# Kernel optimization log

Measured on AMD Instinct MI355X. Metric: run time of the kernel, lower is better.

The kernel has to match this reference:

```python
import jax, jax.numpy as jnp
import numpy as np

N_WIN = 232
T = 8
KERNEL = (2, 2, 2)
STRIDE = (2, 2, 2)
SLOPE = 25.0  # fast_sigmoid surrogate slope


@jax.custom_vjp
def spike(v):
    # heaviside(v) with fast-sigmoid surrogate gradient
    return (v > 0).astype(v.dtype)

def _spike_fwd(v):
    return spike(v), v

def _spike_bwd(v, g):
    return (g / (SLOPE * jnp.abs(v) + 1.0) ** 2,)

spike.defvjp(_spike_fwd, _spike_bwd)


def _avg_pool3d(x, kernel, stride):
    # x: (B, C, D, H, W), VALID pooling
    win = (1, 1) + tuple(kernel)
    st = (1, 1) + tuple(stride)
    s = jax.lax.reduce_window(x, 0.0, jax.lax.add, win, st, 'VALID')
    return s / float(np.prod(kernel))


def setup_inputs() -> dict:
    key = jax.random.key(0)
    ks = jax.random.split(key, 14)
    B, C, H, W = 64, 3, 32, 32
    input_dim, h0, h1, n_cls = 256, 256, 128, 6
    x = jax.random.normal(ks[0], (B, C, N_WIN, H, W), jnp.float32)
    W_in = jax.random.normal(ks[1], (h0, input_dim), jnp.float32) * 0.05
    b_in = jnp.zeros((h0,), jnp.float32)
    W_hid = jax.random.normal(ks[2], (h1, h0), jnp.float32) * 0.05
    b_hid = jnp.zeros((h1,), jnp.float32)
    in_feat = C * h1 * 14  # C * hidden[1] * D'
    W_out = jax.random.normal(ks[3], (n_cls, in_feat), jnp.float32) * 0.05
    b_out = jnp.zeros((n_cls,), jnp.float32)
    beta_in = jax.random.uniform(ks[4], (h0,), jnp.float32)
    thr_in = jax.random.uniform(ks[5], (h0,), jnp.float32)
    beta_hid = jax.random.uniform(ks[6], (h1,), jnp.float32)
    thr_hid = jax.random.uniform(ks[7], (h1,), jnp.float32)
    beta_out = jax.random.uniform(ks[8], (n_cls,), jnp.float32)
    return dict(x=x, W_in=W_in, b_in=b_in, W_hid=W_hid, b_hid=b_hid,
                W_out=W_out, b_out=b_out, beta_in=beta_in, thr_in=thr_in,
                beta_hid=beta_hid, thr_hid=thr_hid, beta_out=beta_out)


def _lif(mem, cur, beta, thr):
    # snntorch Leaky, reset-by-subtract; reset uses detached prev-mem spike
    reset = jax.lax.stop_gradient((mem > thr).astype(mem.dtype))
    mem = jnp.clip(beta, 0.0, 1.0) * mem + cur - reset * thr
    spk = spike(mem - thr)
    return spk, mem


def reference(x, W_in, b_in, W_hid, b_hid, W_out, b_out,
              beta_in, thr_in, beta_hid, thr_hid, beta_out):
    B, C, _, H, W = x.shape
    chunk = N_WIN // T  # 29
    # split depth into T chunks: (T, B, C, chunk, H, W)
    xt = x.reshape(B, C, T, chunk, H, W).transpose(2, 0, 1, 3, 4, 5)
    pooled = jax.vmap(lambda v: _avg_pool3d(v, KERNEL, STRIDE))(xt)  # (T,B,C,D',H',W')
    _, _, _, Dp, Hp, Wp = pooled.shape
    pr = pooled.reshape(T, B, C * Dp, Hp * Wp)
    # fc_in applied to all timesteps at once (recurrence-free)
    cur_in_all = jnp.einsum('tbnf,hf->tbnh', pr, W_in) + b_in  # (T,B,N,h0)

    h0 = W_in.shape[0]
    h1 = W_hid.shape[0]
    n_cls = W_out.shape[0]
    N = C * Dp
    mem_in0 = jnp.zeros((B, N, h0), x.dtype)
    mem_hid0 = jnp.zeros((B, N, h1), x.dtype)
    mem_out0 = jnp.zeros((B, n_cls), x.dtype)

    def step(carry, cur_in):
        mem_in, mem_hid, mem_out = carry
        spk_in, mem_in = _lif(mem_in, cur_in, beta_in, thr_in)
        cur_hid = jnp.einsum('bnh,gh->bng', spk_in, W_hid) + b_hid
        spk_hid, mem_hid = _lif(mem_hid, cur_hid, beta_hid, thr_hid)
        flat = spk_hid.reshape(spk_hid.shape[0], -1)  # (B, N*h1)
        cur_out = flat @ W_out.T + b_out
        spk_out, mem_out = _lif(mem_out, cur_out, beta_out, jnp.float32(1.0))
        return (mem_in, mem_hid, mem_out), spk_out

    _, spk_rec = jax.lax.scan(step, (mem_in0, mem_hid0, mem_out0), cur_in_all)
    return spk_rec  # (T, B, n_classes)
```

## Files before the change

kernel.cpp:

```cpp
#include <hip/hip_runtime.h>

#define T_STEPS 8
#define NROW    42
#define BN      2688
#define H0      256
#define H1      128
#define NCLS    6
#define KFLAT   5376

__global__ __launch_bounds__(256) void pool_kernel(const float* __restrict__ x,
                                                   float* __restrict__ pr) {
    int idx = blockIdx.x * 256 + threadIdx.x;
    int f   = idx & 255;
    int wp  = f & 15, hp = f >> 4;
    int rest = idx >> 8;
    int dp = rest % 14;
    int r2 = rest / 14;
    int c  = r2 % 3;
    int r3 = r2 / 3;
    int b  = r3 & 63;
    int t  = r3 >> 6;
    const float* base = x + ((long)b * 712704 + (long)c * 237568
                          + (long)(t * 29 + 2 * dp) * 1024
                          + (2 * hp) * 32 + 2 * wp);
    float2 v0 = *(const float2*)(base);
    float2 v1 = *(const float2*)(base + 32);
    float2 v2 = *(const float2*)(base + 1024);
    float2 v3 = *(const float2*)(base + 1056);
    float s = v0.x + v0.y + v1.x + v1.y + v2.x + v2.y + v3.x + v3.y;
    int m = t * BN + b * NROW + c * 14 + dp;
    pr[(long)m * 256 + f] = s * 0.125f;
}

__global__ __launch_bounds__(256) void gemm_abt(const float* __restrict__ A,
                                                const float* __restrict__ B,
                                                const float* __restrict__ bias,
                                                float* __restrict__ C,
                                                int N, int K) {
    __shared__ float At[16][68];
    __shared__ float Bt[16][68];
    int tid = threadIdx.x;
    int m0 = blockIdx.y * 64, n0 = blockIdx.x * 64;
    int lr = tid >> 2;
    int lq = tid & 3;
    int tm = tid & 15, tn = tid >> 4;
    float acc[4][4] = {};
    const float* Ap = A + (long)(m0 + lr) * K + lq * 4;
    const float* Bp = B + (long)(n0 + lr) * K + lq * 4;
    for (int k0 = 0; k0 < K; k0 += 16) {
        float4 a = *(const float4*)(Ap + k0);
        float4 b = *(const float4*)(Bp + k0);
        __syncthreads();
        At[lq * 4 + 0][lr] = a.x; At[lq * 4 + 1][lr] = a.y;
        At[lq * 4 + 2][lr] = a.z; At[lq * 4 + 3][lr] = a.w;
        Bt[lq * 4 + 0][lr] = b.x; Bt[lq * 4 + 1][lr] = b.y;
        Bt[lq * 4 + 2][lr] = b.z; Bt[lq * 4 + 3][lr] = b.w;
        __syncthreads();
#pragma unroll
        for (int k = 0; k < 16; ++k) {
            float4 av = *(const float4*)&At[k][tm * 4];
            float4 bv = *(const float4*)&Bt[k][tn * 4];
            float am[4] = {av.x, av.y, av.z, av.w};
            float bn_[4] = {bv.x, bv.y, bv.z, bv.w};
#pragma unroll
            for (int i = 0; i < 4; ++i)
#pragma unroll
                for (int j = 0; j < 4; ++j)
                    acc[i][j] = fmaf(am[i], bn_[j], acc[i][j]);
        }
    }
#pragma unroll
    for (int i = 0; i < 4; ++i) {
        int row = m0 + tm * 4 + i;
        int col = n0 + tn * 4;
        float4 o;
        o.x = acc[i][0] + bias[col + 0];
        o.y = acc[i][1] + bias[col + 1];
        o.z = acc[i][2] + bias[col + 2];
        o.w = acc[i][3] + bias[col + 3];
        *(float4*)&C[(long)row * N + col] = o;
    }
}

__global__ __launch_bounds__(256) void lif_kernel(const float* __restrict__ cur_all,
                                                  const float* __restrict__ beta,
                                                  const float* __restrict__ thr,
                                                  float* __restrict__ spk_all,
                                                  int F) {
    int j = blockIdx.x * 256 + threadIdx.x;
    int h = j & (F - 1);
    float be = fminf(fmaxf(beta[h], 0.f), 1.f);
    float th = thr[h];
    float mem = 0.f;
    long stride = (long)BN * F;
#pragma unroll
    for (int t = 0; t < T_STEPS; ++t) {
        float cur = cur_all[t * stride + j];
        float reset = (mem > th) ? th : 0.f;
        mem = be * mem + cur - reset;
        spk_all[t * stride + j] = ((mem - th) > 0.f) ? 1.f : 0.f;
    }
}

__global__ __launch_bounds__(256) void out_gemm(const float* __restrict__ spkh,
                                                const float* __restrict__ W_out,
                                                const float* __restrict__ b_out,
                                                float* __restrict__ cur_out) {
    __shared__ float part[256][8];
    int row = blockIdx.x;
    int tid = threadIdx.x;
    const float* a = spkh + (long)row * KFLAT;
    float acc[6] = {0.f, 0.f, 0.f, 0.f, 0.f, 0.f};
    for (int j = tid; j < KFLAT; j += 256) {
        float s = a[j];
#pragma unroll
        for (int c = 0; c < 6; ++c)
            acc[c] = fmaf(s, W_out[c * KFLAT + j], acc[c]);
    }
#pragma unroll
    for (int c = 0; c < 6; ++c) part[tid][c] = acc[c];
    __syncthreads();
    for (int off = 128; off > 0; off >>= 1) {
        if (tid < off) {
#pragma unroll
            for (int c = 0; c < 6; ++c) part[tid][c] += part[tid + off][c];
        }
        __syncthreads();
    }
    if (tid < 6) cur_out[row * 6 + tid] = part[0][tid] + b_out[tid];
}

__global__ void lif_out_kernel(const float* __restrict__ cur_out,
                               const float* __restrict__ beta_out,
                               float* __restrict__ out) {
    int j = threadIdx.x;
    if (j >= 384) return;
    int cls = j % 6;
    float be = fminf(fmaxf(beta_out[cls], 0.f), 1.f);
    float mem = 0.f;
#pragma unroll
    for (int t = 0; t < T_STEPS; ++t) {
        float cur = cur_out[t * 384 + j];
        float reset = (mem > 1.f) ? 1.f : 0.f;
        mem = be * mem + cur - reset;
        out[t * 384 + j] = ((mem - 1.f) > 0.f) ? 1.f : 0.f;
    }
}

extern "C" void kernel_launch(void* const* d_in, const int* in_sizes, int n_in,
                              void* d_out, int out_size, void* d_ws, size_t ws_size,
                              hipStream_t stream) {
    (void)in_sizes; (void)n_in; (void)out_size; (void)ws_size;
    const float* x        = (const float*)d_in[0];
    const float* W_in     = (const float*)d_in[1];
    const float* b_in     = (const float*)d_in[2];
    const float* W_hid    = (const float*)d_in[3];
    const float* b_hid    = (const float*)d_in[4];
    const float* W_out    = (const float*)d_in[5];
    const float* b_out    = (const float*)d_in[6];
    const float* beta_in  = (const float*)d_in[7];
    const float* thr_in   = (const float*)d_in[8];
    const float* beta_hid = (const float*)d_in[9];
    const float* thr_hid  = (const float*)d_in[10];
    const float* beta_out = (const float*)d_in[11];
    float* out = (float*)d_out;

    float* buf0 = (float*)d_ws;
    float* buf1 = buf0 + 5505024;
    float* curo = buf1 + 5505024;

    pool_kernel<<<21504, 256, 0, stream>>>(x, buf0);
    gemm_abt<<<dim3(4, 336), 256, 0, stream>>>(buf0, W_in, b_in, buf1, 256, 256);
    lif_kernel<<<2688, 256, 0, stream>>>(buf1, beta_in, thr_in, buf0, 256);
    gemm_abt<<<dim3(2, 336), 256, 0, stream>>>(buf0, W_hid, b_hid, buf1, 128, 256);
    lif_kernel<<<1344, 256, 0, stream>>>(buf1, beta_hid, thr_hid, buf0, 128);
    out_gemm<<<512, 256, 0, stream>>>(buf0, W_out, b_out, curo);
    lif_out_kernel<<<1, 384, 0, stream>>>(curo, beta_out, out);
}
```

Baseline: 377.1 us.

## Enlarge GEMM tiles to 128x128 with 8x8 register blocking and swizzled LDS

The shared fp32 GEMM used for fc_in and fc_hid now computes 128x128 output tiles per block, with each thread holding an 8x8 accumulator instead of 4x4. Each LDS element is therefore reused more per load, reducing shared-memory traffic per FMA. A small row swizzle in LDS is added to avoid bank conflicts on the transposed stores, and launch_bounds requests 4 blocks per CU. The cost is far fewer blocks: 336 for the first GEMM and only 168 for the second, which may underfill the GPU. The 64-entry accumulator also raises register pressure.

New measurement: 402.1 us. +6.6%, slower.

```diff
diff --git a/kernel.cpp b/kernel.cpp
--- a/kernel.cpp
+++ b/kernel.cpp
@@ -7,6 +7,9 @@
 #define H1      128
 #define NCLS    6
 #define KFLAT   5376
+
+#define SW(r)   ((r) + ((r) >> 5) * 4)
+#define LDR     140
 
 __global__ __launch_bounds__(256) void pool_kernel(const float* __restrict__ x,
                                                    float* __restrict__ pr) {
@@ -32,53 +35,74 @@
     pr[(long)m * 256 + f] = s * 0.125f;
 }
 
-__global__ __launch_bounds__(256) void gemm_abt(const float* __restrict__ A,
-                                                const float* __restrict__ B,
-                                                const float* __restrict__ bias,
-                                                float* __restrict__ C,
-                                                int N, int K) {
-    __shared__ float At[16][68];
-    __shared__ float Bt[16][68];
+__global__ __launch_bounds__(256, 4) void gemm_abt(const float* __restrict__ A,
+                                                   const float* __restrict__ B,
+                                                   const float* __restrict__ bias,
+                                                   float* __restrict__ C,
+                                                   int N, int K) {
+    __shared__ float At[16 * LDR];
+    __shared__ float Bt[16 * LDR];
     int tid = threadIdx.x;
-    int m0 = blockIdx.y * 64, n0 = blockIdx.x * 64;
-    int lr = tid >> 2;
-    int lq = tid & 3;
+    int m0 = blockIdx.y * 128, n0 = blockIdx.x * 128;
+
+    int sr = tid >> 1, sq = tid & 1;
+    int scol = SW(sr);
+    const float* Ap = A + (long)(m0 + sr) * K + sq * 8;
+    const float* Bp = B + (long)(n0 + sr) * K + sq * 8;
+
     int tm = tid & 15, tn = tid >> 4;
-    float acc[4][4] = {};
-    const float* Ap = A + (long)(m0 + lr) * K + lq * 4;
-    const float* Bp = B + (long)(n0 + lr) * K + lq * 4;
+    int ca = SW(tm * 8);
+    int cb = SW(tn * 8);
+
+    float acc[8][8] = {};
+
     for (int k0 = 0; k0 < K; k0 += 16) {
-        float4 a = *(const float4*)(Ap + k0);
-        float4 b = *(const float4*)(Bp + k0);
+        float4 a0 = *(const float4*)(Ap + k0);
+        float4 a1 = *(const float4*)(Ap + k0 + 4);
+        float4 b0 = *(const float4*)(Bp + k0);
+        float4 b1 = *(const float4*)(Bp + k0 + 4);
         __syncthreads();
-        At[lq * 4 + 0][lr] = a.x; At[lq * 4 + 1][lr] = a.y;
-        At[lq * 4 + 2][lr] = a.z; At[lq * 4 + 3][lr] = a.w;
-        Bt[lq * 4 + 0][lr] = b.x; Bt[lq * 4 + 1][lr] = b.y;
-        Bt[lq * 4 + 2][lr] = b.z; Bt[lq * 4 + 3][lr] = b.w;
+        int kb = sq * 8;
+        At[(kb + 0) * LDR + scol] = a0.x; At[(kb + 1) * LDR + scol] = a0.y;
+        At[(kb + 2) * LDR + scol] = a0.z; At[(kb + 3) * LDR + scol] = a0.w;
+        At[(kb + 4) * LDR + scol] = a1.x; At[(kb + 5) * LDR + scol] = a1.y;
+        At[(kb + 6) * LDR + scol] = a1.z; At[(kb + 7) * LDR + scol] = a1.w;
+        Bt[(kb + 0) * LDR + scol] = b0.x; Bt[(kb + 1) * LDR + scol] = b0.y;
+        Bt[(kb + 2) * LDR + scol] = b0.z; Bt[(kb + 3) * LDR + scol] = b0.w;
+        Bt[(kb + 4) * LDR + scol] = b1.x; Bt[(kb + 5) * LDR + scol] = b1.y;
+        Bt[(kb + 6) * LDR + scol] = b1.z; Bt[(kb + 7) * LDR + scol] = b1.w;
         __syncthreads();
 #pragma unroll
         for (int k = 0; k < 16; ++k) {
-            float4 av = *(const float4*)&At[k][tm * 4];
-            float4 bv = *(const float4*)&Bt[k][tn * 4];
-            float am[4] = {av.x, av.y, av.z, av.w};
-            float bn_[4] = {bv.x, bv.y, bv.z, bv.w};
-#pragma unroll
-            for (int i = 0; i < 4; ++i)
-#pragma unroll
-                for (int j = 0; j < 4; ++j)
+            float4 av0 = *(const float4*)&At[k * LDR + ca];
+            float4 av1 = *(const float4*)&At[k * LDR + ca + 4];
+            float4 bv0 = *(const float4*)&Bt[k * LDR + cb];
+            float4 bv1 = *(const float4*)&Bt[k * LDR + cb + 4];
+            float am[8] = {av0.x, av0.y, av0.z, av0.w, av1.x, av1.y, av1.z, av1.w};
+            float bn_[8] = {bv0.x, bv0.y, bv0.z, bv0.w, bv1.x, bv1.y, bv1.z, bv1.w};
+#pragma unroll
+            for (int i = 0; i < 8; ++i)
+#pragma unroll
+                for (int j = 0; j < 8; ++j)
                     acc[i][j] = fmaf(am[i], bn_[j], acc[i][j]);
         }
     }
-#pragma unroll
-    for (int i = 0; i < 4; ++i) {
-        int row = m0 + tm * 4 + i;
-        int col = n0 + tn * 4;
-        float4 o;
-        o.x = acc[i][0] + bias[col + 0];
-        o.y = acc[i][1] + bias[col + 1];
-        o.z = acc[i][2] + bias[col + 2];
-        o.w = acc[i][3] + bias[col + 3];
-        *(float4*)&C[(long)row * N + col] = o;
+
+#pragma unroll
+    for (int i = 0; i < 8; ++i) {
+        int row = m0 + tm * 8 + i;
+        int col = n0 + tn * 8;
+        float4 o0, o1;
+        o0.x = acc[i][0] + bias[col + 0];
+        o0.y = acc[i][1] + bias[col + 1];
+        o0.z = acc[i][2] + bias[col + 2];
+        o0.w = acc[i][3] + bias[col + 3];
+        o1.x = acc[i][4] + bias[col + 4];
+        o1.y = acc[i][5] + bias[col + 5];
+        o1.z = acc[i][6] + bias[col + 6];
+        o1.w = acc[i][7] + bias[col + 7];
+        *(float4*)&C[(long)row * N + col]     = o0;
+        *(float4*)&C[(long)row * N + col + 4] = o1;
     }
 }
 
@@ -170,9 +194,9 @@
     float* curo = buf1 + 5505024;
 
     pool_kernel<<<21504, 256, 0, stream>>>(x, buf0);
-    gemm_abt<<<dim3(4, 336), 256, 0, stream>>>(buf0, W_in, b_in, buf1, 256, 256);
+    gemm_abt<<<dim3(2, 168), 256, 0, stream>>>(buf0, W_in, b_in, buf1, 256, 256);
     lif_kernel<<<2688, 256, 0, stream>>>(buf1, beta_in, thr_in, buf0, 256);
-    gemm_abt<<<dim3(2, 336), 256, 0, stream>>>(buf0, W_hid, b_hid, buf1, 128, 256);
+    gemm_abt<<<dim3(1, 168), 256, 0, stream>>>(buf0, W_hid, b_hid, buf1, 128, 256);
     lif_kernel<<<1344, 256, 0, stream>>>(buf1, beta_hid, thr_hid, buf0, 128);
     out_gemm<<<512, 256, 0, stream>>>(buf0, W_out, b_out, curo);
     lif_out_kernel<<<1, 384, 0, stream>>>(curo, beta_out, out);
```
